# Kernel tuning notes

Hardware: AMD Instinct MI355X
Metric: run time of the kernel (lower is better)

The kernel has to match this reference:

```python
import jax, jax.numpy as jnp
import numpy as np

N = 50000   # num nodes
R = 8       # num relations
E = 800000  # num edges
IN, HID, OUT = 128, 128, 64


def rgcn_layer(x, src, dst, etype, W, root, bias):
    """PyG-style RGCNConv: per-relation mean aggregation + root weight + bias.
    x: [N, I], W: [R, I, O], root: [I, O], bias: [O]."""
    O = W.shape[-1]
    # transform node features once per relation: [R, N, O]
    xr = jnp.einsum('ni,rio->rno', x, W)
    # per-edge message = relation-specific transform of source node
    m = xr[etype, src]                      # [E, O] gather
    # mean-aggregate per (relation, dst) pair, then sum over relations
    idx = etype * N + dst                   # combined segment id in [0, R*N)
    s = jax.ops.segment_sum(m, idx, num_segments=R * N)          # [R*N, O]
    c = jax.ops.segment_sum(jnp.ones_like(etype, dtype=m.dtype), idx,
                            num_segments=R * N)                   # [R*N]
    agg = (s / jnp.maximum(c, 1.0)[:, None]).reshape(R, N, O).sum(axis=0)
    return agg + x @ root + bias


def setup_inputs() -> dict:
    key = jax.random.key(0)
    ks = jax.random.split(key, 16)
    x = jax.random.normal(ks[0], (N, IN), dtype=jnp.float32)
    edge_index = jax.random.randint(ks[1], (2, E), 0, N, dtype=jnp.int32)
    edge_type = jax.random.randint(ks[2], (E,), 0, R, dtype=jnp.int32)
    dims = [(IN, HID), (HID, HID), (HID, HID), (HID, OUT)]
    inp = {"x": x, "edge_index": edge_index, "edge_type": edge_type}
    for li, (i, o) in enumerate(dims):
        sc = 1.0 / np.sqrt(i)
        inp[f"W{li+1}"] = jax.random.normal(ks[3 + 3 * li], (R, i, o), dtype=jnp.float32) * sc
        inp[f"root{li+1}"] = jax.random.normal(ks[4 + 3 * li], (i, o), dtype=jnp.float32) * sc
        inp[f"b{li+1}"] = jnp.zeros((o,), dtype=jnp.float32)
    return inp


def reference(x, edge_index, edge_type,
              W1, root1, b1, W2, root2, b2,
              W3, root3, b3, W4, root4, b4):
    src, dst = edge_index[0], edge_index[1]
    h = jax.nn.relu(rgcn_layer(x, src, dst, edge_type, W1, root1, b1))
    h = jax.nn.relu(rgcn_layer(h, src, dst, edge_type, W2, root2, b2))
    h = jax.nn.relu(rgcn_layer(h, src, dst, edge_type, W3, root3, b3))
    h = rgcn_layer(h, src, dst, edge_type, W4, root4, b4)
    return jax.nn.log_softmax(h, axis=1)
```

## Files before the change

kernel.cpp:

```cpp
#include <hip/hip_runtime.h>
#include <math.h>

#define NN 50000
#define RR 8
#define EE 800000
#define RN 400000
#define DIN 128
#define K1 1024
#define KTOT 1152
#define NBLK 391

#define OFF_U    0UL
#define OFF_HB0  102400000UL
#define OFF_HB1  115200000UL
#define OFF_XB   128000000UL
#define OFF_LG   140800000UL
#define OFF_WT   153600000UL
#define OFF_OFFS 154780160UL
#define OFF_CUR  156380288UL
#define OFF_SRT  157980288UL
#define OFF_BS   161180288UL
#define WS_NEED  161184384UL

typedef short bf16x8 __attribute__((ext_vector_type(8)));
typedef float f32x4 __attribute__((ext_vector_type(4)));

__device__ __forceinline__ unsigned f2bf(float f) {
    unsigned x = __float_as_uint(f);
    return (x + 0x7fffu + ((x >> 16) & 1u)) >> 16;
}
__device__ __forceinline__ float bflo(unsigned p) { return __uint_as_float(p << 16); }
__device__ __forceinline__ float bfhi(unsigned p) { return __uint_as_float(p & 0xffff0000u); }

__global__ void k_cvt(const float* __restrict__ x, ushort* __restrict__ xb) {
    int i = blockIdx.x * 256 + threadIdx.x;
    if (i >= NN * 32) return;
    float4 v = ((const float4*)x)[i];
    ushort4 o;
    o.x = (ushort)f2bf(v.x); o.y = (ushort)f2bf(v.y);
    o.z = (ushort)f2bf(v.z); o.w = (ushort)f2bf(v.w);
    ((ushort4*)xb)[i] = o;
}

__global__ void k_wt(const float* __restrict__ W, const float* __restrict__ Rt,
                     ushort* __restrict__ WT, int O) {
    int o = blockIdx.x;
    for (int k = threadIdx.x; k < KTOT; k += 256) {
        float v = (k < K1)
            ? W[(size_t)(k >> 7) * 128 * O + (size_t)(k & 127) * O + o]
            : Rt[(size_t)(k - K1) * O + o];
        WT[(size_t)o * KTOT + k] = (ushort)f2bf(v);
    }
}

__global__ void k_hist(const int* __restrict__ ei, const int* __restrict__ et,
                       int* __restrict__ hist) {
    int e = blockIdx.x * blockDim.x + threadIdx.x;
    if (e >= EE) return;
    atomicAdd(&hist[ei[EE + e] * RR + et[e]], 1);
}

__global__ void k_scan1(const int* __restrict__ hist, int* __restrict__ offs,
                        int* __restrict__ bsums) {
    __shared__ int tmp[1024];
    int tid = threadIdx.x;
    int g = blockIdx.x * 1024 + tid;
    int v = (g < RN) ? hist[g] : 0;
    tmp[tid] = v;
    __syncthreads();
    for (int off = 1; off < 1024; off <<= 1) {
        int t = tmp[tid];
        if (tid >= off) t += tmp[tid - off];
        __syncthreads();
        tmp[tid] = t;
        __syncthreads();
    }
    if (g < RN) offs[g] = tmp[tid] - v;
    if (tid == 1023) bsums[blockIdx.x] = tmp[1023];
}

__global__ void k_scan2(int* __restrict__ bsums) {
    __shared__ int tmp[1024];
    int tid = threadIdx.x;
    int v = (tid < NBLK) ? bsums[tid] : 0;
    tmp[tid] = v;
    __syncthreads();
    for (int off = 1; off < 1024; off <<= 1) {
        int t = tmp[tid];
        if (tid >= off) t += tmp[tid - off];
        __syncthreads();
        tmp[tid] = t;
        __syncthreads();
    }
    if (tid < NBLK) bsums[tid] = tmp[tid] - v;
}

__global__ void k_scan3(int* __restrict__ offs, const int* __restrict__ bsums) {
    int g = blockIdx.x * 1024 + threadIdx.x;
    if (g < RN) offs[g] += bsums[blockIdx.x];
    else if (g == RN) offs[RN] = EE;
}

__global__ void k_scatter(const int* __restrict__ ei, const int* __restrict__ et,
                          const int* __restrict__ offs, int* __restrict__ cur,
                          int* __restrict__ ssrc) {
    int e = blockIdx.x * blockDim.x + threadIdx.x;
    if (e >= EE) return;
    int s = ei[EE + e] * RR + et[e];
    ssrc[offs[s] + atomicAdd(&cur[s], 1)] = ei[e];
}

__global__ __launch_bounds__(256) void k_agg(const ushort* __restrict__ hb,
        const int* __restrict__ offs, const int* __restrict__ ssrc,
        ushort* __restrict__ u) {
    int gt = blockIdx.x * 256 + threadIdx.x;
    int wid = gt >> 6, lane = gt & 63;
    int nw = (gridDim.x * 256) >> 6;
    int half = lane >> 5;
    int sub = lane & 31;
    const uint2* h4 = (const uint2*)hb;
    uint2* u4 = (uint2*)u;

    if (wid >= NN) return;
    int b_cur = offs[wid * 8 + min(lane, 8)];
    for (int n = wid; n < NN; n += nw) {
        int b0 = __shfl(b_cur, 0);
        int b8 = __shfl(b_cur, 8);
        int nb = b8 - b0;
        int sv = ssrc[min(b0 + min(lane, max(nb - 1, 0)), EE - 1)];
        int b_nxt = 0;
        if (n + nw < NN) b_nxt = offs[(n + nw) * 8 + min(lane, 8)];
#pragma unroll
        for (int t = 0; t < 4; ++t) {
            int r = 2 * t + half;
            int beg = __shfl(b_cur, r);
            int end = __shfl(b_cur, r + 1);
            int len = end - beg;
            int mx = max(__shfl(len, 0), __shfl(len, 32));
            float a0 = 0.f, a1 = 0.f, a2 = 0.f, a3 = 0.f;
            for (int j = 0; j < mx; j += 2) {
                int l0 = beg - b0 + j;
                int l1 = l0 + 1;
                int s0 = __shfl(sv, min(l0, 63));
                int s1 = __shfl(sv, min(l1, 63));
                if (l1 >= 64) {
                    s0 = ssrc[min(b0 + l0, EE - 1)];
                    s1 = ssrc[min(b0 + l1, EE - 1)];
                }
                uint2 q0 = h4[(size_t)s0 * 32 + sub];
                uint2 q1 = h4[(size_t)s1 * 32 + sub];
                if (j < len) {
                    a0 += bflo(q0.x); a1 += bfhi(q0.x);
                    a2 += bflo(q0.y); a3 += bfhi(q0.y);
                }
                if (j + 1 < len) {
                    a0 += bflo(q1.x); a1 += bfhi(q1.x);
                    a2 += bflo(q1.y); a3 += bfhi(q1.y);
                }
            }
            float inv = 1.0f / (float)max(len, 1);
            uint2 w;
            w.x = f2bf(a0 * inv) | (f2bf(a1 * inv) << 16);
            w.y = f2bf(a2 * inv) | (f2bf(a3 * inv) << 16);
            u4[(size_t)(n * 8 + r) * 32 + sub] = w;
        }
        b_cur = b_nxt;
    }
}

template<int NT, bool RELU, bool OUTF32>
__global__ __launch_bounds__(256, 6) void k_gemm(
        const ushort* __restrict__ u, const ushort* __restrict__ hb,
        const ushort* __restrict__ WT, const float* __restrict__ bias,
        void* __restrict__ outv) {
    constexpr int BN = 4 * NT * 16;
    __shared__ ushort As[2][32 * 128];
    const int tid = threadIdx.x;
    const int lane = tid & 63;
    const int wc = tid >> 6;
    const int m0 = blockIdx.x * 32;
    f32x4 acc[2][NT] = {};
    uint4 regs[2];

    auto loadA = [&](int t) {
#pragma unroll
        for (int i = 0; i < 2; ++i) {
            int c = i * 256 + tid;
            int row = c >> 4, g = c & 15;
            int nn = min(m0 + row, NN - 1);
            const ushort* p = (t < 8) ? u + (size_t)nn * 1024 + t * 128 + g * 8
                                      : hb + (size_t)nn * 128 + g * 8;
            regs[i] = *(const uint4*)p;
        }
    };
    auto storeA = [&](int buf) {
#pragma unroll
        for (int i = 0; i < 2; ++i) {
            int c = i * 256 + tid;
            int row = c >> 4, g = c & 15;
            *(uint4*)(&As[buf][row * 128 + ((g ^ (row & 15)) * 8)]) = regs[i];
        }
    };
    auto mma = [&](int t, int buf) {
#pragma unroll
        for (int kk = 0; kk < 4; ++kk) {
            bf16x8 bfr[NT];
#pragma unroll
            for (int nt = 0; nt < NT; ++nt) {
                int col = wc * NT * 16 + nt * 16 + (lane & 15);
                int k = t * 128 + kk * 32 + (lane >> 4) * 8;
                bfr[nt] = *(const bf16x8*)(WT + (size_t)col * KTOT + k);
            }
#pragma unroll
            for (int mt = 0; mt < 2; ++mt) {
                int row = mt * 16 + (lane & 15);
                int g = kk * 4 + (lane >> 4);
                bf16x8 a = *(const bf16x8*)(&As[buf][row * 128 + ((g ^ (row & 15)) * 8)]);
#pragma unroll
                for (int nt = 0; nt < NT; ++nt)
                    acc[mt][nt] = __builtin_amdgcn_mfma_f32_16x16x32_bf16(
                        a, bfr[nt], acc[mt][nt], 0, 0, 0);
            }
        }
    };

    loadA(0);
    storeA(0);
    __syncthreads();
    for (int t = 0; t < 9; ++t) {
        if (t < 8) loadA(t + 1);
        mma(t, t & 1);
        if (t < 8) storeA((t + 1) & 1);
        __syncthreads();
    }
#pragma unroll
    for (int mt = 0; mt < 2; ++mt) {
#pragma unroll
        for (int nt = 0; nt < NT; ++nt) {
            int col = wc * NT * 16 + nt * 16 + (lane & 15);
            float bs = bias[col];
#pragma unroll
            for (int j = 0; j < 4; ++j) {
                int row = m0 + mt * 16 + (lane >> 4) * 4 + j;
                if (row >= NN) continue;
                float v = acc[mt][nt][j] + bs;
                if (RELU) v = fmaxf(v, 0.f);
                if (OUTF32) ((float*)outv)[(size_t)row * BN + col] = v;
                else ((ushort*)outv)[(size_t)row * BN + col] = (ushort)f2bf(v);
            }
        }
    }
}

__global__ void k_logsoftmax(const float* __restrict__ in, float* __restrict__ out) {
    int row = blockIdx.x * 4 + (threadIdx.x >> 6);
    int lane = threadIdx.x & 63;
    if (row >= NN) return;
    float v = in[(size_t)row * 64 + lane];
    float m = v;
#pragma unroll
    for (int off = 32; off; off >>= 1) m = fmaxf(m, __shfl_xor(m, off, 64));
    float e = expf(v - m);
    float s = e;
#pragma unroll
    for (int off = 32; off; off >>= 1) s += __shfl_xor(s, off, 64);
    out[(size_t)row * 64 + lane] = v - m - logf(s);
}

extern "C" void kernel_launch(void* const* d_in, const int* in_sizes, int n_in,
                              void* d_out, int out_size, void* d_ws, size_t ws_size,
                              hipStream_t stream) {
    const float* x  = (const float*)d_in[0];
    const int*   ei = (const int*)d_in[1];
    const int*   et = (const int*)d_in[2];
    const float* W[4]    = {(const float*)d_in[3], (const float*)d_in[6],
                            (const float*)d_in[9], (const float*)d_in[12]};
    const float* root[4] = {(const float*)d_in[4], (const float*)d_in[7],
                            (const float*)d_in[10], (const float*)d_in[13]};
    const float* bias[4] = {(const float*)d_in[5], (const float*)d_in[8],
                            (const float*)d_in[11], (const float*)d_in[14]};

    if (ws_size < WS_NEED) return;

    char* ws = (char*)d_ws;
    ushort* u    = (ushort*)(ws + OFF_U);
    ushort* hb0  = (ushort*)(ws + OFF_HB0);
    ushort* hb1  = (ushort*)(ws + OFF_HB1);
    ushort* xb   = (ushort*)(ws + OFF_XB);
    float*  lg   = (float*)(ws + OFF_LG);
    ushort* WT   = (ushort*)(ws + OFF_WT);
    int*   offs  = (int*)(ws + OFF_OFFS);
    int*   cur   = (int*)(ws + OFF_CUR);
    int*   ssrc  = (int*)(ws + OFF_SRT);
    int*   bsums = (int*)(ws + OFF_BS);
    ushort* WTl[4] = {WT, WT + 147456, WT + 2 * 147456, WT + 3 * 147456};

    k_cvt<<<(NN * 32 + 255) / 256, 256, 0, stream>>>(x, xb);
    k_wt<<<128, 256, 0, stream>>>(W[0], root[0], WTl[0], 128);
    k_wt<<<128, 256, 0, stream>>>(W[1], root[1], WTl[1], 128);
    k_wt<<<128, 256, 0, stream>>>(W[2], root[2], WTl[2], 128);
    k_wt<<<64,  256, 0, stream>>>(W[3], root[3], WTl[3], 64);

    hipMemsetAsync(cur, 0, RN * sizeof(int), stream);
    k_hist<<<(EE + 255) / 256, 256, 0, stream>>>(ei, et, cur);
    k_scan1<<<NBLK, 1024, 0, stream>>>(cur, offs, bsums);
    k_scan2<<<1, 1024, 0, stream>>>(bsums);
    k_scan3<<<NBLK, 1024, 0, stream>>>(offs, bsums);
    hipMemsetAsync(cur, 0, RN * sizeof(int), stream);
    k_scatter<<<(EE + 255) / 256, 256, 0, stream>>>(ei, et, offs, cur, ssrc);

    const int G = (NN + 31) / 32;
    k_agg<<<2048, 256, 0, stream>>>(xb, offs, ssrc, u);
    k_gemm<2, true, false><<<G, 256, 0, stream>>>(u, xb, WTl[0], bias[0], hb0);
    k_agg<<<2048, 256, 0, stream>>>(hb0, offs, ssrc, u);
    k_gemm<2, true, false><<<G, 256, 0, stream>>>(u, hb0, WTl[1], bias[1], hb1);
    k_agg<<<2048, 256, 0, stream>>>(hb1, offs, ssrc, u);
    k_gemm<2, true, false><<<G, 256, 0, stream>>>(u, hb1, WTl[2], bias[2], hb0);
    k_agg<<<2048, 256, 0, stream>>>(hb0, offs, ssrc, u);
    k_gemm<1, false, true><<<G, 256, 0, stream>>>(u, hb0, WTl[3], bias[3], lg);
    k_logsoftmax<<<(NN + 3) / 4, 256, 0, stream>>>(lg, (float*)d_out);
}
```

Before: 611.7 us.

## Restructure GEMM to per-wave row tiles with direct global loads, no LDS

The GEMM kernel drops its LDS double-buffered A tile and barriers. Each wave now owns 32 rows and loads A fragments straight from global memory. The grid becomes 2D, with blocks of 128 rows times 64 output columns, so for 128-wide outputs each A row is read by two blocks. This removes LDS traffic and synchronisation but gives up A sharing across waves, doubles global A reads on the 128-wide layers, and uses uncoalesced 16-byte row fragment loads.

Result: slower. 666.1 us (+8.9%).

```diff
diff --git a/kernel.cpp b/kernel.cpp
--- a/kernel.cpp
+++ b/kernel.cpp
@@ -168,76 +168,69 @@
     }
 }
 
-template<int NT, bool RELU, bool OUTF32>
-__global__ __launch_bounds__(256, 6) void k_gemm(
+template<bool RELU, bool OUTF32>
+__global__ __launch_bounds__(256) void k_gemm(
         const ushort* __restrict__ u, const ushort* __restrict__ hb,
         const ushort* __restrict__ WT, const float* __restrict__ bias,
-        void* __restrict__ outv) {
-    constexpr int BN = 4 * NT * 16;
-    __shared__ ushort As[2][32 * 128];
+        void* __restrict__ outv, int O) {
     const int tid = threadIdx.x;
     const int lane = tid & 63;
-    const int wc = tid >> 6;
-    const int m0 = blockIdx.x * 32;
-    f32x4 acc[2][NT] = {};
-    uint4 regs[2];
-
-    auto loadA = [&](int t) {
-#pragma unroll
-        for (int i = 0; i < 2; ++i) {
-            int c = i * 256 + tid;
-            int row = c >> 4, g = c & 15;
-            int nn = min(m0 + row, NN - 1);
-            const ushort* p = (t < 8) ? u + (size_t)nn * 1024 + t * 128 + g * 8
-                                      : hb + (size_t)nn * 128 + g * 8;
-            regs[i] = *(const uint4*)p;
-        }
-    };
-    auto storeA = [&](int buf) {
-#pragma unroll
-        for (int i = 0; i < 2; ++i) {
-            int c = i * 256 + tid;
-            int row = c >> 4, g = c & 15;
-            *(uint4*)(&As[buf][row * 128 + ((g ^ (row & 15)) * 8)]) = regs[i];
-        }
-    };
-    auto mma = [&](int t, int buf) {
+    const int w = tid >> 6;
+    const int m0 = blockIdx.x * 128 + w * 32;
+    const int o0 = blockIdx.y * 64;
+    const int lr = lane & 15;
+    const int lk = (lane >> 4) * 8;
+    f32x4 acc[2][4] = {};
+
+    const ushort* arow[2];
+#pragma unroll
+    for (int mt = 0; mt < 2; ++mt)
+        arow[mt] = u + (size_t)min(m0 + mt * 16 + lr, NN - 1) * 1024;
+    const ushort* wcol[4];
+#pragma unroll
+    for (int nt = 0; nt < 4; ++nt)
+        wcol[nt] = WT + (size_t)(o0 + nt * 16 + lr) * KTOT;
+
+#pragma unroll
+    for (int t = 0; t < 8; ++t) {
 #pragma unroll
         for (int kk = 0; kk < 4; ++kk) {
-            bf16x8 bfr[NT];
-#pragma unroll
-            for (int nt = 0; nt < NT; ++nt) {
-                int col = wc * NT * 16 + nt * 16 + (lane & 15);
-                int k = t * 128 + kk * 32 + (lane >> 4) * 8;
-                bfr[nt] = *(const bf16x8*)(WT + (size_t)col * KTOT + k);
+            bf16x8 a[2];
+#pragma unroll
+            for (int mt = 0; mt < 2; ++mt)
+                a[mt] = *(const bf16x8*)(arow[mt] + t * 128 + kk * 32 + lk);
+#pragma unroll
+            for (int nt = 0; nt < 4; ++nt) {
+                bf16x8 b = *(const bf16x8*)(wcol[nt] + t * 128 + kk * 32 + lk);
+#pragma unroll
+                for (int mt = 0; mt < 2; ++mt)
+                    acc[mt][nt] = __builtin_amdgcn_mfma_f32_16x16x32_bf16(
+                        a[mt], b, acc[mt][nt], 0, 0, 0);
             }
-#pragma unroll
-            for (int mt = 0; mt < 2; ++mt) {
-                int row = mt * 16 + (lane & 15);
-                int g = kk * 4 + (lane >> 4);
-                bf16x8 a = *(const bf16x8*)(&As[buf][row * 128 + ((g ^ (row & 15)) * 8)]);
-#pragma unroll
-                for (int nt = 0; nt < NT; ++nt)
-                    acc[mt][nt] = __builtin_amdgcn_mfma_f32_16x16x32_bf16(
-                        a, bfr[nt], acc[mt][nt], 0, 0, 0);
-            }
-        }
-    };
-
-    loadA(0);
-    storeA(0);
-    __syncthreads();
-    for (int t = 0; t < 9; ++t) {
-        if (t < 8) loadA(t + 1);
-        mma(t, t & 1);
-        if (t < 8) storeA((t + 1) & 1);
-        __syncthreads();
+        }
+    }
+#pragma unroll
+    for (int kk = 0; kk < 4; ++kk) {
+        bf16x8 a[2];
+#pragma unroll
+        for (int mt = 0; mt < 2; ++mt) {
+            int n = min(m0 + mt * 16 + lr, NN - 1);
+            a[mt] = *(const bf16x8*)(hb + (size_t)n * 128 + kk * 32 + lk);
+        }
+#pragma unroll
+        for (int nt = 0; nt < 4; ++nt) {
+            bf16x8 b = *(const bf16x8*)(wcol[nt] + K1 + kk * 32 + lk);
+#pragma unroll
+            for (int mt = 0; mt < 2; ++mt)
+                acc[mt][nt] = __builtin_amdgcn_mfma_f32_16x16x32_bf16(
+                    a[mt], b, acc[mt][nt], 0, 0, 0);
+        }
     }
 #pragma unroll
     for (int mt = 0; mt < 2; ++mt) {
 #pragma unroll
-        for (int nt = 0; nt < NT; ++nt) {
-            int col = wc * NT * 16 + nt * 16 + (lane & 15);
+        for (int nt = 0; nt < 4; ++nt) {
+            int col = o0 + nt * 16 + lr;
             float bs = bias[col];
 #pragma unroll
             for (int j = 0; j < 4; ++j) {
@@ -245,8 +238,8 @@
                 if (row >= NN) continue;
                 float v = acc[mt][nt][j] + bs;
                 if (RELU) v = fmaxf(v, 0.f);
-                if (OUTF32) ((float*)outv)[(size_t)row * BN + col] = v;
-                else ((ushort*)outv)[(size_t)row * BN + col] = (ushort)f2bf(v);
+                if (OUTF32) ((float*)outv)[(size_t)row * O + col] = v;
+                else ((ushort*)outv)[(size_t)row * O + col] = (ushort)f2bf(v);
             }
         }
     }
@@ -309,14 +302,14 @@
     hipMemsetAsync(cur, 0, RN * sizeof(int), stream);
     k_scatter<<<(EE + 255) / 256, 256, 0, stream>>>(ei, et, offs, cur, ssrc);
 
-    const int G = (NN + 31) / 32;
+    const dim3 G2(391, 2), G1(391, 1);
     k_agg<<<2048, 256, 0, stream>>>(xb, offs, ssrc, u);
-    k_gemm<2, true, false><<<G, 256, 0, stream>>>(u, xb, WTl[0], bias[0], hb0);
+    k_gemm<true, false><<<G2, 256, 0, stream>>>(u, xb, WTl[0], bias[0], hb0, 128);
     k_agg<<<2048, 256, 0, stream>>>(hb0, offs, ssrc, u);
-    k_gemm<2, true, false><<<G, 256, 0, stream>>>(u, hb0, WTl[1], bias[1], hb1);
+    k_gemm<true, false><<<G2, 256, 0, stream>>>(u, hb0, WTl[1], bias[1], hb1, 128);
     k_agg<<<2048, 256, 0, stream>>>(hb1, offs, ssrc, u);
-    k_gemm<2, true, false><<<G, 256, 0, stream>>>(u, hb1, WTl[2], bias[2], hb0);
+    k_gemm<true, false><<<G2, 256, 0, stream>>>(u, hb1, WTl[2], bias[2], hb0, 128);
     k_agg<<<2048, 256, 0, stream>>>(hb0, offs, ssrc, u);
-    k_gemm<1, false, true><<<G, 256, 0, stream>>>(u, hb0, WTl[3], bias[3], lg);
+    k_gemm<false, true><<<G1, 256, 0, stream>>>(u, hb0, WTl[3], bias[3], lg, 64);
     k_logsoftmax<<<(NN + 3) / 4, 256, 0, stream>>>(lg, (float*)d_out);
 }
```
